# Performance work log

Hardware: AMD Instinct MI355X
Metric: run time of the kernel (lower is better)

Reference implementation:

```python
import jax, jax.numpy as jnp
import numpy as np

B, S, H = 4, 8192, 768
E, K = 8, 2


def setup_inputs() -> dict:
    key = jax.random.key(0)
    ks = jax.random.split(key, 5)
    scale = 1.0 / np.sqrt(H)
    x = jax.random.normal(ks[0], (B, S, H), dtype=jnp.float32)
    router_w = jax.random.uniform(ks[1], (E, H), jnp.float32, -scale, scale)   # torch Linear(h, E).weight
    router_b = jax.random.uniform(ks[2], (E,), jnp.float32, -scale, scale)
    expert_w = jax.random.uniform(ks[3], (E, H, H), jnp.float32, -scale, scale)  # [E, out, in]
    expert_b = jax.random.uniform(ks[4], (E, H), jnp.float32, -scale, scale)
    return {"x": x, "router_w": router_w, "router_b": router_b,
            "expert_w": expert_w, "expert_b": expert_b}


def reference(x, router_w, router_b, expert_w, expert_b):
    # Router: scores [b,s,E] -> softmax -> top-k probs/ids
    scores = jnp.einsum('bsh,eh->bse', x, router_w) + router_b
    probs = jax.nn.softmax(scores, axis=-1)
    top_probs, expert_ids = jax.lax.top_k(probs, K)          # [b,s,K]
    # Dense grouped expert linears: y[b,s,e,d] = x[b,s,:] @ W_e.T + b_e
    y = jnp.einsum('bsh,edh->bsed', x, expert_w) + expert_b   # [b,s,E,H]
    # Gather the k selected experts' outputs per token
    out_k = jnp.take_along_axis(y, expert_ids[..., None], axis=2)  # [b,s,K,H]
    # Normalize top-k probs and combine
    w = top_probs / (jnp.sum(top_probs, axis=-1, keepdims=True) + 1e-9)  # [b,s,K]
    out = jnp.einsum('bsk,bskh->bsh', w, out_k)
    return out
```

## Files before the change

kernel.cpp:

```cpp
#include <hip/hip_runtime.h>
#include <stdint.h>

#define TOK 32768
#define H 768
#define NE 8
#define CAP 8192
#define BM 128
#define BN 128
#define BK 32

typedef __bf16 bf16x8 __attribute__((ext_vector_type(8)));
typedef float  f32x4  __attribute__((ext_vector_type(4)));

#define OFF_ASSIGN 256
#define OFF_L0 (OFF_ASSIGN + TOK*16)
#define OFF_W0 (OFF_L0 + NE*CAP*4)
#define OFF_L1 (OFF_W0 + NE*CAP*4)
#define OFF_W1 (OFF_L1 + NE*CAP*4)
#define OFF_XB (OFF_W1 + NE*CAP*4)
#define OFF_WB (OFF_XB + (size_t)TOK*H*2)

__device__ __forceinline__ unsigned short f2bf(float f) {
    uint32_t u = __builtin_bit_cast(uint32_t, f);
    u = (u + 0x7fffu + ((u >> 16) & 1u)) >> 16;
    return (unsigned short)u;
}

__device__ __forceinline__ void async_cp16(const void* g, void* l) {
    __builtin_amdgcn_global_load_lds(
        (const __attribute__((address_space(1))) void*)g,
        (__attribute__((address_space(3))) void*)l, 16, 0, 0);
}

__global__ __launch_bounds__(256) void convert_w(const float* __restrict__ src,
                                                 unsigned short* __restrict__ dst, int n4) {
    int i = blockIdx.x * 256 + threadIdx.x;
    if (i < n4) {
        float4 v = ((const float4*)src)[i];
        ushort4 h;
        h.x = f2bf(v.x); h.y = f2bf(v.y); h.z = f2bf(v.z); h.w = f2bf(v.w);
        ((ushort4*)dst)[i] = h;
    }
}

__global__ __launch_bounds__(256) void router_kernel(
    const float* __restrict__ x, const float* __restrict__ rw, const float* __restrict__ rb,
    unsigned short* __restrict__ xb, int4* __restrict__ assign)
{
    int wid  = threadIdx.x >> 6;
    int lane = threadIdx.x & 63;
    int token = blockIdx.x * 4 + wid;

    const float4* xr  = (const float4*)(x + (size_t)token * H);
    const float4* rw4 = (const float4*)rw;

    float s[NE];
    #pragma unroll
    for (int e = 0; e < NE; e++) s[e] = 0.f;

    #pragma unroll
    for (int i = 0; i < 3; i++) {
        int p = lane + 64 * i;
        float4 xv = xr[p];
        ushort4 xh;
        xh.x = f2bf(xv.x); xh.y = f2bf(xv.y); xh.z = f2bf(xv.z); xh.w = f2bf(xv.w);
        ((ushort4*)(xb + (size_t)token * H))[p] = xh;
        #pragma unroll
        for (int e = 0; e < NE; e++) {
            float4 wv = rw4[e * 192 + p];
            s[e] += xv.x * wv.x + xv.y * wv.y + xv.z * wv.z + xv.w * wv.w;
        }
    }
    #pragma unroll
    for (int e = 0; e < NE; e++) {
        float v = s[e];
        #pragma unroll
        for (int off = 32; off; off >>= 1) v += __shfl_xor(v, off, 64);
        s[e] = v + rb[e];
    }
    if (lane == 0) {
        int e0 = 0;
        #pragma unroll
        for (int e = 1; e < NE; e++) if (s[e] > s[e0]) e0 = e;
        int e1 = -1;
        #pragma unroll
        for (int e = 0; e < NE; e++) {
            if (e == e0) continue;
            if (e1 < 0 || s[e] > s[e1]) e1 = e;
        }
        float mx = s[e0];
        float Z = 0.f;
        #pragma unroll
        for (int e = 0; e < NE; e++) Z += __expf(s[e] - mx);
        float p0 = __expf(s[e0] - mx) / Z;
        float p1 = __expf(s[e1] - mx) / Z;
        float inv = 1.f / (p0 + p1 + 1e-9f);
        int4 a;
        a.x = e0; a.y = e1;
        a.z = __float_as_int(p0 * inv);
        a.w = __float_as_int(p1 * inv);
        assign[token] = a;
    }
}

#define SCAT_T 1024
__global__ __launch_bounds__(256) void scatter_kernel(
    const int4* __restrict__ assign, int* __restrict__ counts,
    int* __restrict__ l0, float* __restrict__ w0,
    int* __restrict__ l1, float* __restrict__ w1)
{
    __shared__ int lcnt[2 * NE];
    __shared__ int lbase[2 * NE];
    int tid = threadIdx.x;
    if (tid < 2 * NE) lcnt[tid] = 0;
    __syncthreads();

    int4 a[SCAT_T / 256];
    int  r0[SCAT_T / 256], r1[SCAT_T / 256];
    #pragma unroll
    for (int j = 0; j < SCAT_T / 256; j++) {
        int token = blockIdx.x * SCAT_T + j * 256 + tid;
        a[j] = assign[token];
        r0[j] = atomicAdd(&lcnt[a[j].x], 1);
        r1[j] = atomicAdd(&lcnt[NE + a[j].y], 1);
    }
    __syncthreads();
    if (tid < 2 * NE) lbase[tid] = atomicAdd(&counts[tid], lcnt[tid]);
    __syncthreads();

    #pragma unroll
    for (int j = 0; j < SCAT_T / 256; j++) {
        int token = blockIdx.x * SCAT_T + j * 256 + tid;
        int p0 = lbase[a[j].x] + r0[j];
        int p1 = lbase[NE + a[j].y] + r1[j];
        l0[a[j].x * CAP + p0] = token; w0[a[j].x * CAP + p0] = __int_as_float(a[j].z);
        l1[a[j].y * CAP + p1] = token; w1[a[j].y * CAP + p1] = __int_as_float(a[j].w);
    }
}

#define PIN() __builtin_amdgcn_sched_barrier(0)

template <bool ACCUM>
__global__ __launch_bounds__(256) void expert_gemm(
    const unsigned short* __restrict__ xb, const unsigned short* __restrict__ wb,
    const float* __restrict__ eb, const int* __restrict__ counts,
    const int* __restrict__ lists, const float* __restrict__ wlists,
    float* __restrict__ out)
{
    int bid = blockIdx.x;
    int e   = bid & 7;
    int q   = bid >> 3;
    int n0  = (q % 6) * BN;
    int m0  = (q / 6) * BM;
    int cnt = counts[e];
    if (m0 >= cnt) return;

    __shared__ unsigned short As[3][BM * BK];
    __shared__ unsigned short Bs[3][BN * BK];
    __shared__ int   toks[BM];
    __shared__ float wts[BM];

    int tid = threadIdx.x;
    if (tid < BM) {
        int g = m0 + tid;
        int t = 0; float w = 0.f;
        if (g < cnt) { t = lists[e * CAP + g]; w = wlists[e * CAP + g]; }
        toks[tid] = t; wts[tid] = w;
    }
    __syncthreads();

    int wid = tid >> 6, lane = tid & 63;
    int wm = wid & 1, wn = wid >> 1;
    int quad = lane >> 4, r16 = lane & 15;

    int sr = lane >> 2;
    int cs = (lane & 3) * 8;
    int srow = wid * 16 + sr;

    const unsigned short* gA0 = xb + (size_t)toks[srow]      * H + cs;
    const unsigned short* gA1 = xb + (size_t)toks[64 + srow] * H + cs;
    const unsigned short* gB0 = wb + ((size_t)e * H + n0 + srow)      * H + cs;
    const unsigned short* gB1 = wb + ((size_t)e * H + n0 + 64 + srow) * H + cs;
    char* dA = (char*)&As[0][0] + wid * 1024;
    char* dB = (char*)&Bs[0][0] + wid * 1024;

    f32x4 acc[4][4] = {};

#define STAGE(buf, kel) do { int _bo = (buf) * 8192;      \
    async_cp16(gA0 + (kel), dA + _bo);                    \
    async_cp16(gA1 + (kel), dA + _bo + 4096);             \
    async_cp16(gB0 + (kel), dB + _bo);                    \
    async_cp16(gB1 + (kel), dB + _bo + 4096); } while (0)

#define COMPUTE(t) do {                                                          \
    const unsigned short* Ac = &As[(t) % 3][0];                                  \
    const unsigned short* Bc = &Bs[(t) % 3][0];                                  \
    bf16x8 a[4], b[4];                                                           \
    _Pragma("unroll")                                                            \
    for (int mi = 0; mi < 4; mi++)                                               \
        a[mi] = *(const bf16x8*)(Ac + (wm * 64 + mi * 16 + r16) * BK + quad * 8);\
    _Pragma("unroll")                                                            \
    for (int ni = 0; ni < 4; ni++)                                               \
        b[ni] = *(const bf16x8*)(Bc + (wn * 64 + ni * 16 + r16) * BK + quad * 8);\
    _Pragma("unroll")                                                            \
    for (int mi = 0; mi < 4; mi++)                                               \
        _Pragma("unroll")                                                        \
        for (int ni = 0; ni < 4; ni++)                                           \
            acc[mi][ni] = __builtin_amdgcn_mfma_f32_16x16x32_bf16(               \
                a[mi], b[ni], acc[mi][ni], 0, 0, 0);                             \
} while (0)

#define BOUNDARY(N) do {                                      \
    asm volatile("s_waitcnt vmcnt(" #N ")" ::: "memory");     \
    PIN();                                                    \
    __builtin_amdgcn_s_barrier();                             \
    PIN();                                                    \
    asm volatile("" ::: "memory");                            \
} while (0)

    constexpr int NT = H / BK;
    STAGE(0, 0);
    STAGE(1, BK);
    BOUNDARY(0);

    for (int t = 0; t < NT - 2; t++) {
        STAGE((t + 2) % 3, (t + 2) * BK);
        COMPUTE(t);
        BOUNDARY(4);
    }
    COMPUTE(NT - 2);
    BOUNDARY(0);
    COMPUTE(NT - 1);
#undef STAGE
#undef COMPUTE
#undef BOUNDARY

    float bias[4];
    #pragma unroll
    for (int ni = 0; ni < 4; ni++)
        bias[ni] = eb[e * H + n0 + wn * 64 + ni * 16 + r16];

    #pragma unroll
    for (int mi = 0; mi < 4; mi++) {
        int rowb = wm * 64 + mi * 16 + quad * 4;
        #pragma unroll
        for (int r = 0; r < 4; r++) {
            int row = rowb + r;
            if (m0 + row < cnt) {
                float w = wts[row];
                float* orow = out + (size_t)toks[row] * H + n0 + wn * 64;
                #pragma unroll
                for (int ni = 0; ni < 4; ni++) {
                    float v = (acc[mi][ni][r] + bias[ni]) * w;
                    if (ACCUM) v += orow[ni * 16 + r16];
                    orow[ni * 16 + r16] = v;
                }
            }
        }
    }
}

extern "C" void kernel_launch(void* const* d_in, const int* in_sizes, int n_in,
                              void* d_out, int out_size, void* d_ws, size_t ws_size,
                              hipStream_t stream) {
    const float* x   = (const float*)d_in[0];
    const float* rw  = (const float*)d_in[1];
    const float* rb  = (const float*)d_in[2];
    const float* ew  = (const float*)d_in[3];
    const float* ebv = (const float*)d_in[4];
    float* out = (float*)d_out;

    char* ws = (char*)d_ws;
    int*   counts = (int*)ws;
    int4*  assign = (int4*)(ws + OFF_ASSIGN);
    int*   l0     = (int*)(ws + OFF_L0);
    float* w0     = (float*)(ws + OFF_W0);
    int*   l1     = (int*)(ws + OFF_L1);
    float* w1     = (float*)(ws + OFF_W1);
    unsigned short* xb = (unsigned short*)(ws + OFF_XB);
    unsigned short* wb = (unsigned short*)(ws + OFF_WB);

    hipMemsetAsync(counts, 0, 64, stream);

    int n4 = NE * H * H / 4;
    convert_w<<<(n4 + 255) / 256, 256, 0, stream>>>(ew, wb, n4);
    router_kernel<<<TOK / 4, 256, 0, stream>>>(x, rw, rb, xb, assign);
    scatter_kernel<<<TOK / SCAT_T, 256, 0, stream>>>(assign, counts, l0, w0, l1, w1);

    int nblk = NE * (H / BN) * (CAP / BM);
    expert_gemm<false><<<nblk, 256, 0, stream>>>(xb, wb, ebv, counts,      l0, w0, out);
    expert_gemm<true ><<<nblk, 256, 0, stream>>>(xb, wb, ebv, counts + NE, l1, w1, out);
}
```

Before: 366.0 us.

## Enlarge expert GEMM tiles to 256x256 with 4-stage pipeline and fuse weight conversion

The expert GEMM now uses 256x256 output tiles with 512 threads and 8x4 MFMA accumulators per wave. Staging moves from triple to quad buffering (128KB LDS), with wait counts adjusted to keep three stages in flight. The aim is more operand reuse per byte loaded and deeper latency hiding. The separate bf16 weight-conversion kernel is folded into the router kernel as extra blocks to save a launch and let the two overlap. The trade-offs are fewer, larger tiles that waste more work on ragged per-expert tails and worse wave balance across CUs, and LDS usage that likely allows only one block per CU.

New measurement: 374.4 us. 2.3% more time.

```diff
diff --git a/kernel.cpp b/kernel.cpp
--- a/kernel.cpp
+++ b/kernel.cpp
@@ -5,8 +5,8 @@
 #define H 768
 #define NE 8
 #define CAP 8192
-#define BM 128
-#define BN 128
+#define BM 256
+#define BN 256
 #define BK 32
 
 typedef __bf16 bf16x8 __attribute__((ext_vector_type(8)));
@@ -32,21 +32,26 @@
         (__attribute__((address_space(3))) void*)l, 16, 0, 0);
 }
 
-__global__ __launch_bounds__(256) void convert_w(const float* __restrict__ src,
-                                                 unsigned short* __restrict__ dst, int n4) {
-    int i = blockIdx.x * 256 + threadIdx.x;
-    if (i < n4) {
-        float4 v = ((const float4*)src)[i];
-        ushort4 h;
-        h.x = f2bf(v.x); h.y = f2bf(v.y); h.z = f2bf(v.z); h.w = f2bf(v.w);
-        ((ushort4*)dst)[i] = h;
-    }
-}
-
-__global__ __launch_bounds__(256) void router_kernel(
+#define RBLK (TOK / 4)
+#define CBLK ((NE * H * H / 4 + 255) / 256)
+
+__global__ __launch_bounds__(256) void router_convert(
     const float* __restrict__ x, const float* __restrict__ rw, const float* __restrict__ rb,
-    unsigned short* __restrict__ xb, int4* __restrict__ assign)
+    unsigned short* __restrict__ xb, int4* __restrict__ assign,
+    const float* __restrict__ ew, unsigned short* __restrict__ wbuf)
 {
+    if (blockIdx.x >= RBLK) {
+        int i = (blockIdx.x - RBLK) * 256 + threadIdx.x;
+        int n4 = NE * H * H / 4;
+        if (i < n4) {
+            float4 v = ((const float4*)ew)[i];
+            ushort4 h;
+            h.x = f2bf(v.x); h.y = f2bf(v.y); h.z = f2bf(v.z); h.w = f2bf(v.w);
+            ((ushort4*)wbuf)[i] = h;
+        }
+        return;
+    }
+
     int wid  = threadIdx.x >> 6;
     int lane = threadIdx.x & 63;
     int token = blockIdx.x * 4 + wid;
@@ -139,9 +144,11 @@
 }
 
 #define PIN() __builtin_amdgcn_sched_barrier(0)
+#define NBUF 4
+#define BUFB 32768
 
 template <bool ACCUM>
-__global__ __launch_bounds__(256) void expert_gemm(
+__global__ __launch_bounds__(512, 2) void expert_gemm(
     const unsigned short* __restrict__ xb, const unsigned short* __restrict__ wb,
     const float* __restrict__ eb, const int* __restrict__ counts,
     const int* __restrict__ lists, const float* __restrict__ wlists,
@@ -150,13 +157,12 @@
     int bid = blockIdx.x;
     int e   = bid & 7;
     int q   = bid >> 3;
-    int n0  = (q % 6) * BN;
-    int m0  = (q / 6) * BM;
+    int n0  = (q % 3) * BN;
+    int m0  = (q / 3) * BM;
     int cnt = counts[e];
     if (m0 >= cnt) return;
 
-    __shared__ unsigned short As[3][BM * BK];
-    __shared__ unsigned short Bs[3][BN * BK];
+    __shared__ char  lds[NBUF * BUFB];
     __shared__ int   toks[BM];
     __shared__ float wts[BM];
 
@@ -173,41 +179,41 @@
     int wm = wid & 1, wn = wid >> 1;
     int quad = lane >> 4, r16 = lane & 15;
 
-    int sr = lane >> 2;
-    int cs = (lane & 3) * 8;
+    int sr   = lane >> 2;
+    int cs   = (lane & 3) * 8;
     int srow = wid * 16 + sr;
 
-    const unsigned short* gA0 = xb + (size_t)toks[srow]      * H + cs;
-    const unsigned short* gA1 = xb + (size_t)toks[64 + srow] * H + cs;
-    const unsigned short* gB0 = wb + ((size_t)e * H + n0 + srow)      * H + cs;
-    const unsigned short* gB1 = wb + ((size_t)e * H + n0 + 64 + srow) * H + cs;
-    char* dA = (char*)&As[0][0] + wid * 1024;
-    char* dB = (char*)&Bs[0][0] + wid * 1024;
-
-    f32x4 acc[4][4] = {};
-
-#define STAGE(buf, kel) do { int _bo = (buf) * 8192;      \
+    const unsigned short* gA0 = xb + (size_t)toks[srow]       * H + cs;
+    const unsigned short* gA1 = xb + (size_t)toks[128 + srow] * H + cs;
+    const unsigned short* gB0 = wb + ((size_t)e * H + n0 + srow)       * H + cs;
+    const unsigned short* gB1 = wb + ((size_t)e * H + n0 + 128 + srow) * H + cs;
+    char* dA = lds + wid * 1024;
+    char* dB = lds + 16384 + wid * 1024;
+
+    f32x4 acc[8][4] = {};
+
+#define STAGE(buf, kel) do { int _bo = (buf) * BUFB;      \
     async_cp16(gA0 + (kel), dA + _bo);                    \
-    async_cp16(gA1 + (kel), dA + _bo + 4096);             \
+    async_cp16(gA1 + (kel), dA + _bo + 8192);             \
     async_cp16(gB0 + (kel), dB + _bo);                    \
-    async_cp16(gB1 + (kel), dB + _bo + 4096); } while (0)
-
-#define COMPUTE(t) do {                                                          \
-    const unsigned short* Ac = &As[(t) % 3][0];                                  \
-    const unsigned short* Bc = &Bs[(t) % 3][0];                                  \
-    bf16x8 a[4], b[4];                                                           \
-    _Pragma("unroll")                                                            \
-    for (int mi = 0; mi < 4; mi++)                                               \
-        a[mi] = *(const bf16x8*)(Ac + (wm * 64 + mi * 16 + r16) * BK + quad * 8);\
-    _Pragma("unroll")                                                            \
-    for (int ni = 0; ni < 4; ni++)                                               \
-        b[ni] = *(const bf16x8*)(Bc + (wn * 64 + ni * 16 + r16) * BK + quad * 8);\
-    _Pragma("unroll")                                                            \
-    for (int mi = 0; mi < 4; mi++)                                               \
-        _Pragma("unroll")                                                        \
-        for (int ni = 0; ni < 4; ni++)                                           \
-            acc[mi][ni] = __builtin_amdgcn_mfma_f32_16x16x32_bf16(               \
-                a[mi], b[ni], acc[mi][ni], 0, 0, 0);                             \
+    async_cp16(gB1 + (kel), dB + _bo + 8192); } while (0)
+
+#define COMPUTE(t) do {                                                           \
+    const unsigned short* Ac = (const unsigned short*)(lds + ((t) & 3) * BUFB);   \
+    const unsigned short* Bc = Ac + 8192;                                         \
+    bf16x8 a[8], b[4];                                                            \
+    _Pragma("unroll")                                                             \
+    for (int mi = 0; mi < 8; mi++)                                                \
+        a[mi] = *(const bf16x8*)(Ac + (wm * 128 + mi * 16 + r16) * BK + quad * 8);\
+    _Pragma("unroll")                                                             \
+    for (int ni = 0; ni < 4; ni++)                                                \
+        b[ni] = *(const bf16x8*)(Bc + (wn * 64 + ni * 16 + r16) * BK + quad * 8); \
+    _Pragma("unroll")                                                             \
+    for (int mi = 0; mi < 8; mi++)                                                \
+        _Pragma("unroll")                                                         \
+        for (int ni = 0; ni < 4; ni++)                                            \
+            acc[mi][ni] = __builtin_amdgcn_mfma_f32_16x16x32_bf16(                \
+                a[mi], b[ni], acc[mi][ni], 0, 0, 0);                              \
 } while (0)
 
 #define BOUNDARY(N) do {                                      \
@@ -221,13 +227,16 @@
     constexpr int NT = H / BK;
     STAGE(0, 0);
     STAGE(1, BK);
+    STAGE(2, 2 * BK);
     BOUNDARY(0);
 
-    for (int t = 0; t < NT - 2; t++) {
-        STAGE((t + 2) % 3, (t + 2) * BK);
+    for (int t = 0; t < NT - 3; t++) {
+        STAGE((t + 3) & 3, (t + 3) * BK);
         COMPUTE(t);
-        BOUNDARY(4);
-    }
+        BOUNDARY(8);
+    }
+    COMPUTE(NT - 3);
+    BOUNDARY(4);
     COMPUTE(NT - 2);
     BOUNDARY(0);
     COMPUTE(NT - 1);
@@ -241,8 +250,8 @@
         bias[ni] = eb[e * H + n0 + wn * 64 + ni * 16 + r16];
 
     #pragma unroll
-    for (int mi = 0; mi < 4; mi++) {
-        int rowb = wm * 64 + mi * 16 + quad * 4;
+    for (int mi = 0; mi < 8; mi++) {
+        int rowb = wm * 128 + mi * 16 + quad * 4;
         #pragma unroll
         for (int r = 0; r < 4; r++) {
             int row = rowb + r;
@@ -282,12 +291,10 @@
 
     hipMemsetAsync(counts, 0, 64, stream);
 
-    int n4 = NE * H * H / 4;
-    convert_w<<<(n4 + 255) / 256, 256, 0, stream>>>(ew, wb, n4);
-    router_kernel<<<TOK / 4, 256, 0, stream>>>(x, rw, rb, xb, assign);
+    router_convert<<<RBLK + CBLK, 256, 0, stream>>>(x, rw, rb, xb, assign, ew, wb);
     scatter_kernel<<<TOK / SCAT_T, 256, 0, stream>>>(assign, counts, l0, w0, l1, w1);
 
     int nblk = NE * (H / BN) * (CAP / BM);
-    expert_gemm<false><<<nblk, 256, 0, stream>>>(xb, wb, ebv, counts,      l0, w0, out);
-    expert_gemm<true ><<<nblk, 256, 0, stream>>>(xb, wb, ebv, counts + NE, l1, w1, out);
-}
+    expert_gemm<false><<<nblk, 512, 0, stream>>>(xb, wb, ebv, counts,      l0, w0, out);
+    expert_gemm<true ><<<nblk, 512, 0, stream>>>(xb, wb, ebv, counts + NE, l1, w1, out);
+}
```
